# Kernel tuning notes

Measured on AMD Instinct MI355X. Metric: run time of the kernel, lower is better.

Reference implementation:

```python
import jax, jax.numpy as jnp
import numpy as np

FP16_MIN = -65504.0  # torch.finfo(torch.float16).min


def addcoords(x):
    # x: (b, c, h, w) NCHW. AddCoords(rank=1, with_r=True): appends a
    # y-coordinate channel (normalized over h, broadcast over w) and |y-0.5|.
    b, c, h, w = x.shape
    yy = (jnp.arange(h, dtype=x.dtype) / (h - 1)) * 2.0 - 1.0  # (h,)
    yy = jnp.broadcast_to(yy[None, None, :, None], (b, 1, h, w))
    rr = jnp.abs(yy - 0.5)
    return jnp.concatenate([x, yy, rr], axis=1)


def conv1x1(x, W, b):
    # W: (c_out, c_in), b: (c_out,)
    return jnp.einsum('bihw,oi->bohw', x, W) + b[None, :, None, None]


def setup_inputs() -> dict:
    key = jax.random.key(0)
    ks = jax.random.split(key, 16)
    c = 64
    B2, h, w = 4, 256, 256
    s_in = 0.02
    inp = {
        'x': jax.random.normal(ks[0], (B2, c, h, w), jnp.float32),
        'res_enc': jax.random.normal(ks[1], (B2, c, h, w), jnp.float32),
        'tr_feat': jax.random.normal(ks[2], (B2, c, h, w), jnp.float32),
        # CoordConv 1x1 weights take c+2 input channels (coord + r channels)
        'Wl1': jax.random.normal(ks[3], (c, c + 2), jnp.float32) * s_in,
        'bl1': jax.random.normal(ks[4], (c,), jnp.float32) * s_in,
        'Wr1': jax.random.normal(ks[5], (c, c + 2), jnp.float32) * s_in,
        'br1': jax.random.normal(ks[6], (c,), jnp.float32) * s_in,
        'Wl2': jax.random.normal(ks[7], (c, c), jnp.float32) * s_in,
        'bl2': jax.random.normal(ks[8], (c,), jnp.float32) * s_in,
        'Wr2': jax.random.normal(ks[9], (c, c), jnp.float32) * s_in,
        'br2': jax.random.normal(ks[10], (c,), jnp.float32) * s_in,
        'beta1': jax.random.normal(ks[11], (1, c, 1, 1), jnp.float32) * s_in,
        'gamma1': jax.random.normal(ks[12], (1, c, 1, 1), jnp.float32) * s_in,
        'beta3': jax.random.normal(ks[13], (1, c, 1, 1), jnp.float32) * s_in,
        'gamma3': jax.random.normal(ks[14], (1, c, 1, 1), jnp.float32) * s_in,
    }
    return inp


def reference(x, res_enc, tr_feat, Wl1, bl1, Wr1, br1, Wl2, bl2, Wr2, br2,
              beta1, gamma1, beta3, gamma3):
    x_l, x_r = jnp.split(x, 2, axis=0)
    re_l, re_r = jnp.split(res_enc, 2, axis=0)
    tr_l, tr_r = jnp.split(tr_feat, 2, axis=0)
    b, c, h, w = x_l.shape
    scale = jnp.asarray(c, x.dtype) ** -0.5

    Q = conv1x1(addcoords(x_l), Wl1, bl1) + beta1 * tr_l   # (b, c, h, w)
    S = conv1x1(addcoords(x_r), Wr1, br1) + beta1 * tr_r   # (b, c, h, w)

    # per-row (epipolar) attention along width: score[b,h,i,j]
    score = jnp.einsum('bchi,bchj->bhij', Q, S) * scale
    idx = jnp.arange(w)
    upper = idx[None, :] > idx[:, None]  # strict upper triangle (j > i)
    score = jnp.where(upper[None, None], FP16_MIN, score)
    # In torch, score_T is a view of score; after in-place masking, score_T
    # masked at strict-lower positions == transpose of masked score.
    M_r2l = jax.nn.softmax(score, axis=-1)                       # (b,h,w,w)
    M_l2r = jax.nn.softmax(jnp.swapaxes(score, -1, -2), axis=-1)  # (b,h,w,w)

    buf_R = conv1x1(x_r, Wr2, br2) + gamma1 * re_r  # (b, c, h, w)
    buf_l = jnp.einsum('bhij,bchj->bchi', M_r2l, buf_R)
    buf_L = conv1x1(x_l, Wl2, bl2) + gamma1 * re_l
    buf_r = jnp.einsum('bhij,bchj->bchi', M_l2r, buf_L)

    out_L = x_l + beta3 * buf_l
    out_R = x_r + gamma3 * buf_r
    return jnp.concatenate([out_L, out_R], axis=0)
```

## Files before the change

### kernel.cpp

```cpp
#include <hip/hip_runtime.h>
#include <stdint.h>

#define HW 65536
#define C_ 64

typedef __attribute__((ext_vector_type(8))) short short8;
typedef __attribute__((ext_vector_type(4))) float f32x4;
typedef long long i64;

#define MFMA16(a, b, c) __builtin_amdgcn_mfma_f32_16x16x32_bf16((a), (b), (c), 0, 0, 0)
#define MFMA8(a, b, c)  __builtin_amdgcn_mfma_f32_16x16x32_fp8_fp8((a), (b), (c), 0, 0, 0)

union U16x8 { uint4 q; short8 v; uint32_t u[4]; };
union PU { uint32_t u[2]; i64 q; };

__device__ inline uint32_t pack_bf16(float lo, float hi) {
  uint32_t ul = __float_as_uint(lo), uh = __float_as_uint(hi);
  ul = (ul + 0x7fffu + ((ul >> 16) & 1u)) >> 16;
  uh = (uh + 0x7fffu + ((uh >> 16) & 1u)) >> 16;
  return ul | (uh << 16);
}
__device__ inline short8 ld8bf(const uint16_t* p) {
  U16x8 t; t.q = *(const uint4*)p; return t.v;
}
__device__ inline i64 ld8f8(const uint8_t* p) { return *(const i64*)p; }
__device__ inline uint32_t pk4f8(float a, float b, float c, float d) {
  uint32_t v = __builtin_amdgcn_cvt_pk_fp8_f32(a, b, 0, false);
  v = __builtin_amdgcn_cvt_pk_fp8_f32(c, d, v, true);
  return v;
}

__device__ inline int qf_idx(int p, int c) { return p * 64 + (c ^ ((p & 7) << 3)); }
__device__ inline int vf_idx(int c, int j) { return c * 256 + (j ^ ((c & 7) << 3)); }
__device__ inline int wf_idx(int r, int k) { return r * 64 + (k ^ ((r & 7) << 3)); }

__global__ __launch_bounds__(512, 2) void SCAM_73151882985874_kernel(
    const float* __restrict__ x, const float* __restrict__ res_enc,
    const float* __restrict__ tr_feat,
    const float* __restrict__ Wl1, const float* __restrict__ bl1,
    const float* __restrict__ Wr1, const float* __restrict__ br1,
    const float* __restrict__ Wl2, const float* __restrict__ bl2,
    const float* __restrict__ Wr2, const float* __restrict__ br2,
    const float* __restrict__ beta1, const float* __restrict__ gamma1,
    const float* __restrict__ beta3, const float* __restrict__ gamma3,
    float* __restrict__ out)
{
  __shared__ __align__(16) uint8_t sQ[16384];
  __shared__ __align__(16) uint8_t sS[16384];
  __shared__ __align__(16) uint8_t sVL[16384];
  __shared__ __align__(16) uint8_t sVR[16384];
  __shared__ __align__(16) uint16_t sW[16384];

  const int tid = threadIdx.x;
  const int wid = tid >> 6, lane = tid & 63, g = lane >> 4, li = lane & 15;
  const int bb = blockIdx.x >> 8, hh = blockIdx.x & 255;
  const float yy = (float)hh * (2.0f / 255.0f) - 1.0f;
  const float rr = fabsf(yy - 0.5f);

  const size_t rowoff = (size_t)hh * 256;
  const float* xl  = x + ((size_t)bb * C_) * HW + rowoff;
  const float* xr  = x + ((size_t)(2 + bb) * C_) * HW + rowoff;
  const float* trl = tr_feat + ((size_t)bb * C_) * HW + rowoff;
  const float* trr = tr_feat + ((size_t)(2 + bb) * C_) * HW + rowoff;
  const float* rel = res_enc + ((size_t)bb * C_) * HW + rowoff;
  const float* rer = res_enc + ((size_t)(2 + bb) * C_) * HW + rowoff;
  float* outL = out + ((size_t)bb * C_) * HW + rowoff;
  float* outR = out + ((size_t)(2 + bb) * C_) * HW + rowoff;

  {
    const int r = tid >> 3, k0 = (tid & 7) * 8;
    const float* Ws[4] = {Wl1, Wr1, Wl2, Wr2};
    const int ldws[4] = {66, 66, 64, 64};
    #pragma unroll
    for (int m = 0; m < 4; ++m) {
      const float* src = Ws[m] + (size_t)r * ldws[m] + k0;
      U16x8 t8;
      t8.u[0] = pack_bf16(src[0], src[1]); t8.u[1] = pack_bf16(src[2], src[3]);
      t8.u[2] = pack_bf16(src[4], src[5]); t8.u[3] = pack_bf16(src[6], src[7]);
      *(uint4*)&sW[m * 4096 + wf_idx(r, k0)] = t8.q;
    }
  }

  const int addr_lo = ((((g & 1) << 1) << 4) + li) << 2;
  const int addr_hi = addr_lo + 64;
  const bool hiD = (g >= 2);

  auto ldXfrag = [&](const float* __restrict__ src, int pix, int c0) -> short8 {
    const float* s = src + (size_t)c0 * HW + pix;
    U16x8 t8;
    t8.u[0] = pack_bf16(s[0],              s[(size_t)HW]);
    t8.u[1] = pack_bf16(s[2 * (size_t)HW], s[3 * (size_t)HW]);
    t8.u[2] = pack_bf16(s[4 * (size_t)HW], s[5 * (size_t)HW]);
    t8.u[3] = pack_bf16(s[6 * (size_t)HW], s[7 * (size_t)HW]);
    return t8.v;
  };

  auto conv_one = [&](int widx, const float* __restrict__ Wc,
                      const float* __restrict__ bias, const float* __restrict__ mod,
                      const float* __restrict__ E,
                      const short8 bx[2][2], uint8_t* dstQS, uint8_t* dstV) {
    const uint16_t* wb = sW + widx * 4096;
    #pragma unroll
    for (int ct = 0; ct < 4; ++ct) {
      const int wr = ct * 16 + li;
      short8 af0 = ld8bf(&wb[wf_idx(wr, g * 8)]);
      short8 af1 = ld8bf(&wb[wf_idx(wr, 32 + g * 8)]);
      float be[4], md[4];
      #pragma unroll
      for (int r = 0; r < 4; ++r) {
        int c = ct * 16 + 4 * g + r;
        float b = bias[c];
        if (Wc) b += Wc[(size_t)c * 66 + 64] * yy + Wc[(size_t)c * 66 + 65] * rr;
        be[r] = b;
        md[r] = mod[c];
      }
      #pragma unroll
      for (int ptl = 0; ptl < 2; ++ptl) {
        int pix = wid * 32 + ptl * 16 + li;
        float ev[4];
        #pragma unroll
        for (int r = 0; r < 4; ++r)
          ev[r] = E[(size_t)(ct * 16 + 4 * g + r) * HW + pix];
        f32x4 acc = {0.f, 0.f, 0.f, 0.f};
        acc = MFMA16(af0, bx[ptl][0], acc);
        acc = MFMA16(af1, bx[ptl][1], acc);
        float v[4];
        #pragma unroll
        for (int r = 0; r < 4; ++r) v[r] = acc[r] + be[r] + md[r] * ev[r];
        if (dstV) {
          uint32_t pk = pk4f8(v[0], v[1], v[2], v[3]);
          #pragma unroll
          for (int r = 0; r < 4; ++r)
            dstV[vf_idx(ct * 16 + 4 * g + r, pix)] = (uint8_t)(pk >> (8 * r));
        } else {
          *(uint32_t*)&dstQS[qf_idx(pix, ct * 16 + 4 * g)] = pk4f8(v[0], v[1], v[2], v[3]);
        }
      }
    }
  };

  {
    short8 bx[2][2];
    #pragma unroll
    for (int ptl = 0; ptl < 2; ++ptl) {
      int pix = wid * 32 + ptl * 16 + li;
      bx[ptl][0] = ldXfrag(xl, pix, g * 8);
      bx[ptl][1] = ldXfrag(xl, pix, 32 + g * 8);
    }
    __syncthreads();
    conv_one(0, Wl1, bl1, beta1,  trl, bx, sQ,  nullptr);
    conv_one(2, nullptr, bl2, gamma1, rel, bx, nullptr, sVL);
  }
  {
    short8 bx[2][2];
    #pragma unroll
    for (int ptl = 0; ptl < 2; ++ptl) {
      int pix = wid * 32 + ptl * 16 + li;
      bx[ptl][0] = ldXfrag(xr, pix, g * 8);
      bx[ptl][1] = ldXfrag(xr, pix, 32 + g * 8);
    }
    conv_one(1, Wr1, br1, beta1,  trr, bx, sS,  nullptr);
    conv_one(3, nullptr, br2, gamma1, rer, bx, nullptr, sVR);
  }
  __syncthreads();

  const int j0 = wid * 32;

  {
    i64 bS00 = ld8f8(&sS[qf_idx(j0 + li, g * 8)]);
    i64 bS01 = ld8f8(&sS[qf_idx(j0 + li, 32 + g * 8)]);
    i64 bS10 = ld8f8(&sS[qf_idx(j0 + 16 + li, g * 8)]);
    i64 bS11 = ld8f8(&sS[qf_idx(j0 + 16 + li, 32 + g * 8)]);
    f32x4 acc[4][2];
    #pragma unroll
    for (int ct = 0; ct < 4; ++ct) { acc[ct][0] = (f32x4){0,0,0,0}; acc[ct][1] = (f32x4){0,0,0,0}; }
    float zp0 = 0.f, zp1 = 0.f;

    for (int ip = wid; ip < 8; ++ip) {
      i64 aQ00 = ld8f8(&sQ[qf_idx(ip * 32 + li, g * 8)]);
      i64 aQ01 = ld8f8(&sQ[qf_idx(ip * 32 + li, 32 + g * 8)]);
      i64 aQ10 = ld8f8(&sQ[qf_idx(ip * 32 + 16 + li, g * 8)]);
      i64 aQ11 = ld8f8(&sQ[qf_idx(ip * 32 + 16 + li, 32 + g * 8)]);
      i64 aV0 = ld8f8(&sVL[vf_idx(li,      ip * 32 + g * 8)]);
      i64 aV1 = ld8f8(&sVL[vf_idx(16 + li, ip * 32 + g * 8)]);
      i64 aV2 = ld8f8(&sVL[vf_idx(32 + li, ip * 32 + g * 8)]);
      i64 aV3 = ld8f8(&sVL[vf_idx(48 + li, ip * 32 + g * 8)]);
      const int a0 = ip * 32 + 4 * g;
      #pragma unroll
      for (int jt = 0; jt < 2; ++jt) {
        const int jj = j0 + jt * 16 + li;
        const i64 b0 = jt ? bS10 : bS00;
        const i64 b1 = jt ? bS11 : bS01;
        f32x4 s0 = {0.f, 0.f, 0.f, 0.f};
        s0 = MFMA8(aQ00, b0, s0); s0 = MFMA8(aQ01, b1, s0);
        f32x4 s1 = {0.f, 0.f, 0.f, 0.f};
        s1 = MFMA8(aQ10, b0, s1); s1 = MFMA8(aQ11, b1, s1);
        float ps = 0.f, p0[4], p1[4];
        #pragma unroll
        for (int r = 0; r < 4; ++r) {
          p0[r] = (a0 + r >= jj)      ? __expf(s0[r] * 0.125f) : 0.f;
          p1[r] = (a0 + 16 + r >= jj) ? __expf(s1[r] * 0.125f) : 0.f;
          ps += p0[r] + p1[r];
        }
        if (jt == 0) zp0 += ps; else zp1 += ps;
        uint32_t D0 = pk4f8(p0[0], p0[1], p0[2], p0[3]);
        uint32_t D1 = pk4f8(p1[0], p1[1], p1[2], p1[3]);
        int w00 = __builtin_amdgcn_ds_bpermute(addr_lo, (int)D0);
        int w01 = __builtin_amdgcn_ds_bpermute(addr_lo, (int)D1);
        int w10 = __builtin_amdgcn_ds_bpermute(addr_hi, (int)D0);
        int w11 = __builtin_amdgcn_ds_bpermute(addr_hi, (int)D1);
        PU t;
        t.u[0] = hiD ? (uint32_t)w01 : (uint32_t)w00;
        t.u[1] = hiD ? (uint32_t)w11 : (uint32_t)w10;
        const i64 bP = t.q;
        acc[0][jt] = MFMA8(aV0, bP, acc[0][jt]);
        acc[1][jt] = MFMA8(aV1, bP, acc[1][jt]);
        acc[2][jt] = MFMA8(aV2, bP, acc[2][jt]);
        acc[3][jt] = MFMA8(aV3, bP, acc[3][jt]);
      }
    }
    zp0 += __shfl_xor(zp0, 16); zp0 += __shfl_xor(zp0, 32);
    zp1 += __shfl_xor(zp1, 16); zp1 += __shfl_xor(zp1, 32);
    #pragma unroll
    for (int jt = 0; jt < 2; ++jt) {
      float invz = 1.0f / (jt == 0 ? zp0 : zp1);
      int j = j0 + jt * 16 + li;
      #pragma unroll
      for (int ct = 0; ct < 4; ++ct)
        #pragma unroll
        for (int r = 0; r < 4; ++r) {
          int c = ct * 16 + 4 * g + r;
          outR[(size_t)c * HW + j] =
              fmaf(gamma3[c], acc[ct][jt][r] * invz, xr[(size_t)c * HW + j]);
        }
    }
  }

  {
    i64 bQ00 = ld8f8(&sQ[qf_idx(j0 + li, g * 8)]);
    i64 bQ01 = ld8f8(&sQ[qf_idx(j0 + li, 32 + g * 8)]);
    i64 bQ10 = ld8f8(&sQ[qf_idx(j0 + 16 + li, g * 8)]);
    i64 bQ11 = ld8f8(&sQ[qf_idx(j0 + 16 + li, 32 + g * 8)]);
    f32x4 acc[4][2];
    #pragma unroll
    for (int ct = 0; ct < 4; ++ct) { acc[ct][0] = (f32x4){0,0,0,0}; acc[ct][1] = (f32x4){0,0,0,0}; }
    float zp0 = 0.f, zp1 = 0.f;

    for (int jp = 0; jp <= wid; ++jp) {
      i64 aS00 = ld8f8(&sS[qf_idx(jp * 32 + li, g * 8)]);
      i64 aS01 = ld8f8(&sS[qf_idx(jp * 32 + li, 32 + g * 8)]);
      i64 aS10 = ld8f8(&sS[qf_idx(jp * 32 + 16 + li, g * 8)]);
      i64 aS11 = ld8f8(&sS[qf_idx(jp * 32 + 16 + li, 32 + g * 8)]);
      i64 aV0 = ld8f8(&sVR[vf_idx(li,      jp * 32 + g * 8)]);
      i64 aV1 = ld8f8(&sVR[vf_idx(16 + li, jp * 32 + g * 8)]);
      i64 aV2 = ld8f8(&sVR[vf_idx(32 + li, jp * 32 + g * 8)]);
      i64 aV3 = ld8f8(&sVR[vf_idx(48 + li, jp * 32 + g * 8)]);
      const int a0 = jp * 32 + 4 * g;
      #pragma unroll
      for (int itl = 0; itl < 2; ++itl) {
        const int ii = j0 + itl * 16 + li;
        const i64 b0 = itl ? bQ10 : bQ00;
        const i64 b1 = itl ? bQ11 : bQ01;
        f32x4 s0 = {0.f, 0.f, 0.f, 0.f};
        s0 = MFMA8(aS00, b0, s0); s0 = MFMA8(aS01, b1, s0);
        f32x4 s1 = {0.f, 0.f, 0.f, 0.f};
        s1 = MFMA8(aS10, b0, s1); s1 = MFMA8(aS11, b1, s1);
        float ps = 0.f, p0[4], p1[4];
        #pragma unroll
        for (int r = 0; r < 4; ++r) {
          p0[r] = (a0 + r <= ii)      ? __expf(s0[r] * 0.125f) : 0.f;
          p1[r] = (a0 + 16 + r <= ii) ? __expf(s1[r] * 0.125f) : 0.f;
          ps += p0[r] + p1[r];
        }
        if (itl == 0) zp0 += ps; else zp1 += ps;
        uint32_t D0 = pk4f8(p0[0], p0[1], p0[2], p0[3]);
        uint32_t D1 = pk4f8(p1[0], p1[1], p1[2], p1[3]);
        int w00 = __builtin_amdgcn_ds_bpermute(addr_lo, (int)D0);
        int w01 = __builtin_amdgcn_ds_bpermute(addr_lo, (int)D1);
        int w10 = __builtin_amdgcn_ds_bpermute(addr_hi, (int)D0);
        int w11 = __builtin_amdgcn_ds_bpermute(addr_hi, (int)D1);
        PU t;
        t.u[0] = hiD ? (uint32_t)w01 : (uint32_t)w00;
        t.u[1] = hiD ? (uint32_t)w11 : (uint32_t)w10;
        const i64 bP = t.q;
        acc[0][itl] = MFMA8(aV0, bP, acc[0][itl]);
        acc[1][itl] = MFMA8(aV1, bP, acc[1][itl]);
        acc[2][itl] = MFMA8(aV2, bP, acc[2][itl]);
        acc[3][itl] = MFMA8(aV3, bP, acc[3][itl]);
      }
    }
    zp0 += __shfl_xor(zp0, 16); zp0 += __shfl_xor(zp0, 32);
    zp1 += __shfl_xor(zp1, 16); zp1 += __shfl_xor(zp1, 32);
    #pragma unroll
    for (int itl = 0; itl < 2; ++itl) {
      float invz = 1.0f / (itl == 0 ? zp0 : zp1);
      int i = j0 + itl * 16 + li;
      #pragma unroll
      for (int ct = 0; ct < 4; ++ct)
        #pragma unroll
        for (int r = 0; r < 4; ++r) {
          int c = ct * 16 + 4 * g + r;
          outL[(size_t)c * HW + i] =
              fmaf(beta3[c], acc[ct][itl][r] * invz, xl[(size_t)c * HW + i]);
        }
    }
  }
}

extern "C" void kernel_launch(void* const* d_in, const int* in_sizes, int n_in,
                              void* d_out, int out_size, void* d_ws, size_t ws_size,
                              hipStream_t stream) {
  const float* x       = (const float*)d_in[0];
  const float* res_enc = (const float*)d_in[1];
  const float* tr_feat = (const float*)d_in[2];
  const float* Wl1     = (const float*)d_in[3];
  const float* bl1     = (const float*)d_in[4];
  const float* Wr1     = (const float*)d_in[5];
  const float* br1     = (const float*)d_in[6];
  const float* Wl2     = (const float*)d_in[7];
  const float* bl2     = (const float*)d_in[8];
  const float* Wr2     = (const float*)d_in[9];
  const float* br2     = (const float*)d_in[10];
  const float* beta1   = (const float*)d_in[11];
  const float* gamma1  = (const float*)d_in[12];
  const float* beta3   = (const float*)d_in[13];
  const float* gamma3  = (const float*)d_in[14];
  float* outp = (float*)d_out;

  dim3 grid(512);
  dim3 block(512);
  SCAM_73151882985874_kernel<<<grid, block, 0, stream>>>(
      x, res_enc, tr_feat, Wl1, bl1, Wr1, br1, Wl2, bl2, Wr2, br2,
      beta1, gamma1, beta3, gamma3, outp);
}
```

Before: 73.32 us.

## Double block to 1024 threads, one 16-pixel tile per wave

Raises the block size from 512 to 1024 threads so each of 16 waves handles one 16-pixel column tile instead of two. Weight staging, the 1x1 convs and both causal attention passes are reorganized around this single-tile-per-wave layout. The goal is more wavefronts in flight to hide global-load and LDS latency, and better balance of the triangular attention work across waves. In exchange, the Q/S/V fragments loaded per iteration are now reused for half as many MFMAs, and 80KB of LDS per block may limit how many blocks fit per CU.

```diff
diff --git a/kernel.cpp b/kernel.cpp
--- a/kernel.cpp
+++ b/kernel.cpp
@@ -34,7 +34,7 @@
 __device__ inline int vf_idx(int c, int j) { return c * 256 + (j ^ ((c & 7) << 3)); }
 __device__ inline int wf_idx(int r, int k) { return r * 64 + (k ^ ((r & 7) << 3)); }
 
-__global__ __launch_bounds__(512, 2) void SCAM_73151882985874_kernel(
+__global__ __launch_bounds__(1024, 4) void SCAM_73151882985874_kernel(
     const float* __restrict__ x, const float* __restrict__ res_enc,
     const float* __restrict__ tr_feat,
     const float* __restrict__ Wl1, const float* __restrict__ bl1,
@@ -68,11 +68,14 @@
   float* outR = out + ((size_t)(2 + bb) * C_) * HW + rowoff;
 
   {
-    const int r = tid >> 3, k0 = (tid & 7) * 8;
+    const int half = tid >> 9;
+    const int t = tid & 511;
+    const int r = t >> 3, k0 = (t & 7) * 8;
     const float* Ws[4] = {Wl1, Wr1, Wl2, Wr2};
     const int ldws[4] = {66, 66, 64, 64};
     #pragma unroll
-    for (int m = 0; m < 4; ++m) {
+    for (int mm = 0; mm < 2; ++mm) {
+      const int m = half + mm * 2;
       const float* src = Ws[m] + (size_t)r * ldws[m] + k0;
       U16x8 t8;
       t8.u[0] = pack_bf16(src[0], src[1]); t8.u[1] = pack_bf16(src[2], src[3]);
@@ -85,7 +88,9 @@
   const int addr_hi = addr_lo + 64;
   const bool hiD = (g >= 2);
 
-  auto ldXfrag = [&](const float* __restrict__ src, int pix, int c0) -> short8 {
+  const int pix = wid * 16 + li;
+
+  auto ldXfrag = [&](const float* __restrict__ src, int c0) -> short8 {
     const float* s = src + (size_t)c0 * HW + pix;
     U16x8 t8;
     t8.u[0] = pack_bf16(s[0],              s[(size_t)HW]);
@@ -98,14 +103,14 @@
   auto conv_one = [&](int widx, const float* __restrict__ Wc,
                       const float* __restrict__ bias, const float* __restrict__ mod,
                       const float* __restrict__ E,
-                      const short8 bx[2][2], uint8_t* dstQS, uint8_t* dstV) {
+                      short8 bx0, short8 bx1, uint8_t* dstQS, uint8_t* dstV) {
     const uint16_t* wb = sW + widx * 4096;
     #pragma unroll
     for (int ct = 0; ct < 4; ++ct) {
       const int wr = ct * 16 + li;
       short8 af0 = ld8bf(&wb[wf_idx(wr, g * 8)]);
       short8 af1 = ld8bf(&wb[wf_idx(wr, 32 + g * 8)]);
-      float be[4], md[4];
+      float be[4], md[4], ev[4];
       #pragma unroll
       for (int r = 0; r < 4; ++r) {
         int c = ct * 16 + 4 * g + r;
@@ -113,70 +118,48 @@
         if (Wc) b += Wc[(size_t)c * 66 + 64] * yy + Wc[(size_t)c * 66 + 65] * rr;
         be[r] = b;
         md[r] = mod[c];
-      }
-      #pragma unroll
-      for (int ptl = 0; ptl < 2; ++ptl) {
-        int pix = wid * 32 + ptl * 16 + li;
-        float ev[4];
+        ev[r] = E[(size_t)c * HW + pix];
+      }
+      f32x4 acc = {0.f, 0.f, 0.f, 0.f};
+      acc = MFMA16(af0, bx0, acc);
+      acc = MFMA16(af1, bx1, acc);
+      float v[4];
+      #pragma unroll
+      for (int r = 0; r < 4; ++r) v[r] = acc[r] + be[r] + md[r] * ev[r];
+      if (dstV) {
+        uint32_t pk = pk4f8(v[0], v[1], v[2], v[3]);
         #pragma unroll
         for (int r = 0; r < 4; ++r)
-          ev[r] = E[(size_t)(ct * 16 + 4 * g + r) * HW + pix];
-        f32x4 acc = {0.f, 0.f, 0.f, 0.f};
-        acc = MFMA16(af0, bx[ptl][0], acc);
-        acc = MFMA16(af1, bx[ptl][1], acc);
-        float v[4];
-        #pragma unroll
-        for (int r = 0; r < 4; ++r) v[r] = acc[r] + be[r] + md[r] * ev[r];
-        if (dstV) {
-          uint32_t pk = pk4f8(v[0], v[1], v[2], v[3]);
-          #pragma unroll
-          for (int r = 0; r < 4; ++r)
-            dstV[vf_idx(ct * 16 + 4 * g + r, pix)] = (uint8_t)(pk >> (8 * r));
-        } else {
-          *(uint32_t*)&dstQS[qf_idx(pix, ct * 16 + 4 * g)] = pk4f8(v[0], v[1], v[2], v[3]);
-        }
+          dstV[vf_idx(ct * 16 + 4 * g + r, pix)] = (uint8_t)(pk >> (8 * r));
+      } else {
+        *(uint32_t*)&dstQS[qf_idx(pix, ct * 16 + 4 * g)] = pk4f8(v[0], v[1], v[2], v[3]);
       }
     }
   };
 
   {
-    short8 bx[2][2];
-    #pragma unroll
-    for (int ptl = 0; ptl < 2; ++ptl) {
-      int pix = wid * 32 + ptl * 16 + li;
-      bx[ptl][0] = ldXfrag(xl, pix, g * 8);
-      bx[ptl][1] = ldXfrag(xl, pix, 32 + g * 8);
-    }
+    short8 bx0 = ldXfrag(xl, g * 8);
+    short8 bx1 = ldXfrag(xl, 32 + g * 8);
     __syncthreads();
-    conv_one(0, Wl1, bl1, beta1,  trl, bx, sQ,  nullptr);
-    conv_one(2, nullptr, bl2, gamma1, rel, bx, nullptr, sVL);
-  }
-  {
-    short8 bx[2][2];
-    #pragma unroll
-    for (int ptl = 0; ptl < 2; ++ptl) {
-      int pix = wid * 32 + ptl * 16 + li;
-      bx[ptl][0] = ldXfrag(xr, pix, g * 8);
-      bx[ptl][1] = ldXfrag(xr, pix, 32 + g * 8);
-    }
-    conv_one(1, Wr1, br1, beta1,  trr, bx, sS,  nullptr);
-    conv_one(3, nullptr, br2, gamma1, rer, bx, nullptr, sVR);
+    conv_one(0, Wl1, bl1, beta1,  trl, bx0, bx1, sQ,  nullptr);
+    conv_one(2, nullptr, bl2, gamma1, rel, bx0, bx1, nullptr, sVL);
+  }
+  {
+    short8 bx0 = ldXfrag(xr, g * 8);
+    short8 bx1 = ldXfrag(xr, 32 + g * 8);
+    conv_one(1, Wr1, br1, beta1,  trr, bx0, bx1, sS,  nullptr);
+    conv_one(3, nullptr, br2, gamma1, rer, bx0, bx1, nullptr, sVR);
   }
   __syncthreads();
 
-  const int j0 = wid * 32;
-
-  {
-    i64 bS00 = ld8f8(&sS[qf_idx(j0 + li, g * 8)]);
-    i64 bS01 = ld8f8(&sS[qf_idx(j0 + li, 32 + g * 8)]);
-    i64 bS10 = ld8f8(&sS[qf_idx(j0 + 16 + li, g * 8)]);
-    i64 bS11 = ld8f8(&sS[qf_idx(j0 + 16 + li, 32 + g * 8)]);
-    f32x4 acc[4][2];
-    #pragma unroll
-    for (int ct = 0; ct < 4; ++ct) { acc[ct][0] = (f32x4){0,0,0,0}; acc[ct][1] = (f32x4){0,0,0,0}; }
-    float zp0 = 0.f, zp1 = 0.f;
-
-    for (int ip = wid; ip < 8; ++ip) {
+  {
+    const int jj = pix;
+    i64 bS0 = ld8f8(&sS[qf_idx(jj, g * 8)]);
+    i64 bS1 = ld8f8(&sS[qf_idx(jj, 32 + g * 8)]);
+    f32x4 acc[4] = {{0,0,0,0},{0,0,0,0},{0,0,0,0},{0,0,0,0}};
+    float z = 0.f;
+
+    for (int ip = (wid >> 1); ip < 8; ++ip) {
       i64 aQ00 = ld8f8(&sQ[qf_idx(ip * 32 + li, g * 8)]);
       i64 aQ01 = ld8f8(&sQ[qf_idx(ip * 32 + li, 32 + g * 8)]);
       i64 aQ10 = ld8f8(&sQ[qf_idx(ip * 32 + 16 + li, g * 8)]);
@@ -185,68 +168,53 @@
       i64 aV1 = ld8f8(&sVL[vf_idx(16 + li, ip * 32 + g * 8)]);
       i64 aV2 = ld8f8(&sVL[vf_idx(32 + li, ip * 32 + g * 8)]);
       i64 aV3 = ld8f8(&sVL[vf_idx(48 + li, ip * 32 + g * 8)]);
+      f32x4 s0 = {0.f, 0.f, 0.f, 0.f};
+      s0 = MFMA8(aQ00, bS0, s0); s0 = MFMA8(aQ01, bS1, s0);
+      f32x4 s1 = {0.f, 0.f, 0.f, 0.f};
+      s1 = MFMA8(aQ10, bS0, s1); s1 = MFMA8(aQ11, bS1, s1);
       const int a0 = ip * 32 + 4 * g;
-      #pragma unroll
-      for (int jt = 0; jt < 2; ++jt) {
-        const int jj = j0 + jt * 16 + li;
-        const i64 b0 = jt ? bS10 : bS00;
-        const i64 b1 = jt ? bS11 : bS01;
-        f32x4 s0 = {0.f, 0.f, 0.f, 0.f};
-        s0 = MFMA8(aQ00, b0, s0); s0 = MFMA8(aQ01, b1, s0);
-        f32x4 s1 = {0.f, 0.f, 0.f, 0.f};
-        s1 = MFMA8(aQ10, b0, s1); s1 = MFMA8(aQ11, b1, s1);
-        float ps = 0.f, p0[4], p1[4];
-        #pragma unroll
-        for (int r = 0; r < 4; ++r) {
-          p0[r] = (a0 + r >= jj)      ? __expf(s0[r] * 0.125f) : 0.f;
-          p1[r] = (a0 + 16 + r >= jj) ? __expf(s1[r] * 0.125f) : 0.f;
-          ps += p0[r] + p1[r];
-        }
-        if (jt == 0) zp0 += ps; else zp1 += ps;
-        uint32_t D0 = pk4f8(p0[0], p0[1], p0[2], p0[3]);
-        uint32_t D1 = pk4f8(p1[0], p1[1], p1[2], p1[3]);
-        int w00 = __builtin_amdgcn_ds_bpermute(addr_lo, (int)D0);
-        int w01 = __builtin_amdgcn_ds_bpermute(addr_lo, (int)D1);
-        int w10 = __builtin_amdgcn_ds_bpermute(addr_hi, (int)D0);
-        int w11 = __builtin_amdgcn_ds_bpermute(addr_hi, (int)D1);
-        PU t;
-        t.u[0] = hiD ? (uint32_t)w01 : (uint32_t)w00;
-        t.u[1] = hiD ? (uint32_t)w11 : (uint32_t)w10;
-        const i64 bP = t.q;
-        acc[0][jt] = MFMA8(aV0, bP, acc[0][jt]);
-        acc[1][jt] = MFMA8(aV1, bP, acc[1][jt]);
-        acc[2][jt] = MFMA8(aV2, bP, acc[2][jt]);
-        acc[3][jt] = MFMA8(aV3, bP, acc[3][jt]);
-      }
-    }
-    zp0 += __shfl_xor(zp0, 16); zp0 += __shfl_xor(zp0, 32);
-    zp1 += __shfl_xor(zp1, 16); zp1 += __shfl_xor(zp1, 32);
-    #pragma unroll
-    for (int jt = 0; jt < 2; ++jt) {
-      float invz = 1.0f / (jt == 0 ? zp0 : zp1);
-      int j = j0 + jt * 16 + li;
-      #pragma unroll
-      for (int ct = 0; ct < 4; ++ct)
-        #pragma unroll
-        for (int r = 0; r < 4; ++r) {
-          int c = ct * 16 + 4 * g + r;
-          outR[(size_t)c * HW + j] =
-              fmaf(gamma3[c], acc[ct][jt][r] * invz, xr[(size_t)c * HW + j]);
-        }
-    }
-  }
-
-  {
-    i64 bQ00 = ld8f8(&sQ[qf_idx(j0 + li, g * 8)]);
-    i64 bQ01 = ld8f8(&sQ[qf_idx(j0 + li, 32 + g * 8)]);
-    i64 bQ10 = ld8f8(&sQ[qf_idx(j0 + 16 + li, g * 8)]);
-    i64 bQ11 = ld8f8(&sQ[qf_idx(j0 + 16 + li, 32 + g * 8)]);
-    f32x4 acc[4][2];
-    #pragma unroll
-    for (int ct = 0; ct < 4; ++ct) { acc[ct][0] = (f32x4){0,0,0,0}; acc[ct][1] = (f32x4){0,0,0,0}; }
-    float zp0 = 0.f, zp1 = 0.f;
-
-    for (int jp = 0; jp <= wid; ++jp) {
+      float p0[4], p1[4];
+      #pragma unroll
+      for (int r = 0; r < 4; ++r) {
+        p0[r] = (a0 + r >= jj)      ? __expf(s0[r] * 0.125f) : 0.f;
+        p1[r] = (a0 + 16 + r >= jj) ? __expf(s1[r] * 0.125f) : 0.f;
+        z += p0[r] + p1[r];
+      }
+      uint32_t D0 = pk4f8(p0[0], p0[1], p0[2], p0[3]);
+      uint32_t D1 = pk4f8(p1[0], p1[1], p1[2], p1[3]);
+      int w00 = __builtin_amdgcn_ds_bpermute(addr_lo, (int)D0);
+      int w01 = __builtin_amdgcn_ds_bpermute(addr_lo, (int)D1);
+      int w10 = __builtin_amdgcn_ds_bpermute(addr_hi, (int)D0);
+      int w11 = __builtin_amdgcn_ds_bpermute(addr_hi, (int)D1);
+      PU t;
+      t.u[0] = hiD ? (uint32_t)w01 : (uint32_t)w00;
+      t.u[1] = hiD ? (uint32_t)w11 : (uint32_t)w10;
+      const i64 bP = t.q;
+      acc[0] = MFMA8(aV0, bP, acc[0]);
+      acc[1] = MFMA8(aV1, bP, acc[1]);
+      acc[2] = MFMA8(aV2, bP, acc[2]);
+      acc[3] = MFMA8(aV3, bP, acc[3]);
+    }
+    z += __shfl_xor(z, 16); z += __shfl_xor(z, 32);
+    float invz = 1.0f / z;
+    #pragma unroll
+    for (int ct = 0; ct < 4; ++ct)
+      #pragma unroll
+      for (int r = 0; r < 4; ++r) {
+        int c = ct * 16 + 4 * g + r;
+        outR[(size_t)c * HW + jj] =
+            fmaf(gamma3[c], acc[ct][r] * invz, xr[(size_t)c * HW + jj]);
+      }
+  }
+
+  {
+    const int ii = pix;
+    i64 bQ0 = ld8f8(&sQ[qf_idx(ii, g * 8)]);
+    i64 bQ1 = ld8f8(&sQ[qf_idx(ii, 32 + g * 8)]);
+    f32x4 acc[4] = {{0,0,0,0},{0,0,0,0},{0,0,0,0},{0,0,0,0}};
+    float z = 0.f;
+
+    for (int jp = 0; jp <= (wid >> 1); ++jp) {
       i64 aS00 = ld8f8(&sS[qf_idx(jp * 32 + li, g * 8)]);
       i64 aS01 = ld8f8(&sS[qf_idx(jp * 32 + li, 32 + g * 8)]);
       i64 aS10 = ld8f8(&sS[qf_idx(jp * 32 + 16 + li, g * 8)]);
@@ -255,55 +223,43 @@
       i64 aV1 = ld8f8(&sVR[vf_idx(16 + li, jp * 32 + g * 8)]);
       i64 aV2 = ld8f8(&sVR[vf_idx(32 + li, jp * 32 + g * 8)]);
       i64 aV3 = ld8f8(&sVR[vf_idx(48 + li, jp * 32 + g * 8)]);
+      f32x4 s0 = {0.f, 0.f, 0.f, 0.f};
+      s0 = MFMA8(aS00, bQ0, s0); s0 = MFMA8(aS01, bQ1, s0);
+      f32x4 s1 = {0.f, 0.f, 0.f, 0.f};
+      s1 = MFMA8(aS10, bQ0, s1); s1 = MFMA8(aS11, bQ1, s1);
       const int a0 = jp * 32 + 4 * g;
-      #pragma unroll
-      for (int itl = 0; itl < 2; ++itl) {
-        const int ii = j0 + itl * 16 + li;
-        const i64 b0 = itl ? bQ10 : bQ00;
-        const i64 b1 = itl ? bQ11 : bQ01;
-        f32x4 s0 = {0.f, 0.f, 0.f, 0.f};
-        s0 = MFMA8(aS00, b0, s0); s0 = MFMA8(aS01, b1, s0);
-        f32x4 s1 = {0.f, 0.f, 0.f, 0.f};
-        s1 = MFMA8(aS10, b0, s1); s1 = MFMA8(aS11, b1, s1);
-        float ps = 0.f, p0[4], p1[4];
-        #pragma unroll
-        for (int r = 0; r < 4; ++r) {
-          p0[r] = (a0 + r <= ii)      ? __expf(s0[r] * 0.125f) : 0.f;
-          p1[r] = (a0 + 16 + r <= ii) ? __expf(s1[r] * 0.125f) : 0.f;
-          ps += p0[r] + p1[r];
-        }
-        if (itl == 0) zp0 += ps; else zp1 += ps;
-        uint32_t D0 = pk4f8(p0[0], p0[1], p0[2], p0[3]);
-        uint32_t D1 = pk4f8(p1[0], p1[1], p1[2], p1[3]);
-        int w00 = __builtin_amdgcn_ds_bpermute(addr_lo, (int)D0);
-        int w01 = __builtin_amdgcn_ds_bpermute(addr_lo, (int)D1);
-        int w10 = __builtin_amdgcn_ds_bpermute(addr_hi, (int)D0);
-        int w11 = __builtin_amdgcn_ds_bpermute(addr_hi, (int)D1);
-        PU t;
-        t.u[0] = hiD ? (uint32_t)w01 : (uint32_t)w00;
-        t.u[1] = hiD ? (uint32_t)w11 : (uint32_t)w10;
-        const i64 bP = t.q;
-        acc[0][itl] = MFMA8(aV0, bP, acc[0][itl]);
-        acc[1][itl] = MFMA8(aV1, bP, acc[1][itl]);
-        acc[2][itl] = MFMA8(aV2, bP, acc[2][itl]);
-        acc[3][itl] = MFMA8(aV3, bP, acc[3][itl]);
-      }
-    }
-    zp0 += __shfl_xor(zp0, 16); zp0 += __shfl_xor(zp0, 32);
-    zp1 += __shfl_xor(zp1, 16); zp1 += __shfl_xor(zp1, 32);
-    #pragma unroll
-    for (int itl = 0; itl < 2; ++itl) {
-      float invz = 1.0f / (itl == 0 ? zp0 : zp1);
-      int i = j0 + itl * 16 + li;
-      #pragma unroll
-      for (int ct = 0; ct < 4; ++ct)
-        #pragma unroll
-        for (int r = 0; r < 4; ++r) {
-          int c = ct * 16 + 4 * g + r;
-          outL[(size_t)c * HW + i] =
-              fmaf(beta3[c], acc[ct][itl][r] * invz, xl[(size_t)c * HW + i]);
-        }
-    }
+      float p0[4], p1[4];
+      #pragma unroll
+      for (int r = 0; r < 4; ++r) {
+        p0[r] = (a0 + r <= ii)      ? __expf(s0[r] * 0.125f) : 0.f;
+        p1[r] = (a0 + 16 + r <= ii) ? __expf(s1[r] * 0.125f) : 0.f;
+        z += p0[r] + p1[r];
+      }
+      uint32_t D0 = pk4f8(p0[0], p0[1], p0[2], p0[3]);
+      uint32_t D1 = pk4f8(p1[0], p1[1], p1[2], p1[3]);
+      int w00 = __builtin_amdgcn_ds_bpermute(addr_lo, (int)D0);
+      int w01 = __builtin_amdgcn_ds_bpermute(addr_lo, (int)D1);
+      int w10 = __builtin_amdgcn_ds_bpermute(addr_hi, (int)D0);
+      int w11 = __builtin_amdgcn_ds_bpermute(addr_hi, (int)D1);
+      PU t;
+      t.u[0] = hiD ? (uint32_t)w01 : (uint32_t)w00;
+      t.u[1] = hiD ? (uint32_t)w11 : (uint32_t)w10;
+      const i64 bP = t.q;
+      acc[0] = MFMA8(aV0, bP, acc[0]);
+      acc[1] = MFMA8(aV1, bP, acc[1]);
+      acc[2] = MFMA8(aV2, bP, acc[2]);
+      acc[3] = MFMA8(aV3, bP, acc[3]);
+    }
+    z += __shfl_xor(z, 16); z += __shfl_xor(z, 32);
+    float invz = 1.0f / z;
+    #pragma unroll
+    for (int ct = 0; ct < 4; ++ct)
+      #pragma unroll
+      for (int r = 0; r < 4; ++r) {
+        int c = ct * 16 + 4 * g + r;
+        outL[(size_t)c * HW + ii] =
+            fmaf(beta3[c], acc[ct][r] * invz, xl[(size_t)c * HW + ii]);
+      }
   }
 }
 
@@ -328,7 +284,7 @@
   float* outp = (float*)d_out;
 
   dim3 grid(512);
-  dim3 block(512);
+  dim3 block(1024);
   SCAM_73151882985874_kernel<<<grid, block, 0, stream>>>(
       x, res_enc, tr_feat, Wl1, bl1, Wr1, br1, Wl2, bl2, Wr2, br2,
       beta1, gamma1, beta3, gamma3, outp);
```

Measured after the change: 112.2 us. +53.0%, slower.
